# Optimization experiments

Hardware: AMD Instinct MI355X
Metric: run time of the kernel (lower is better)

## Reference

```python
import jax, jax.numpy as jnp
import numpy as np

BLOCK_LEN = 64  # chunk length l


def setup_inputs() -> dict:
    key = jax.random.key(0)
    k1, k2, k3 = jax.random.split(key, 3)
    b, s, h, p, n = 8, 4096, 16, 64, 64
    X = jax.random.normal(k1, (b, s, h, p), jnp.float32)
    # A must be negative for numerically stable decays (exp(cumsum diffs) <= 1),
    # matching real Mamba2 where A_log parameterizes a negative decay rate.
    A = -0.1 * jnp.abs(jax.random.normal(k2, (b, s, h), jnp.float32))
    B = jax.random.normal(k3, (b, s, h, n), jnp.float32)
    return {"X": X, "A": A, "B": B}


def reference(X, A, B):
    L = BLOCK_LEN
    b, s, h, p = X.shape
    n = B.shape[-1]
    c = s // L  # number of chunks

    # b (c l) ... -> b c l ...
    Xb = X.reshape(b, c, L, h, p)
    Bb = B.reshape(b, c, L, h, n)
    Ab = jnp.transpose(A.reshape(b, c, L, h), (0, 3, 1, 2))  # (b, h, c, l)

    A_cumsum = jnp.cumsum(Ab, axis=-1)  # (b, h, c, l)

    # Fused decay-einsum: states[b,c,h,p,n] =
    #   sum_l B[b,c,l,h,n] * exp(A_cumsum[b,h,c,-1] - A_cumsum[b,h,c,l]) * X[b,c,l,h,p]
    decay_states = jnp.exp(A_cumsum[..., -1:] - A_cumsum)  # (b, h, c, l)
    states = jnp.einsum('bclhn,bhcl,bclhp->bchpn', Bb, decay_states, Xb)

    # Prepend zero initial states along chunk dim -> (b, c+1, h, p, n)
    states = jnp.concatenate([jnp.zeros_like(states[:, :1]), states], axis=1)

    # Inter-chunk recurrence via exp(segsum(padded chunk totals)).
    padded_A = jnp.pad(A_cumsum[..., -1], ((0, 0), (0, 0), (1, 0)))  # (b, h, c+1)
    cs = jnp.cumsum(padded_A, axis=-1)
    Z = c + 1
    diff = cs[..., :, None] - cs[..., None, :]  # (b, h, Z, Z), row - col
    mask = jnp.tril(jnp.ones((Z, Z), dtype=bool))  # row >= col
    decay_chunk = jnp.where(mask, jnp.exp(diff), 0.0)  # (b, h, Z, Z)

    new_states = jnp.einsum('bhzc,bchpn->bzhpn', decay_chunk, states)
    return new_states[:, -1]  # (b, h, p, n)
```

## Files before the change

kernel.cpp:

```cpp
#include <hip/hip_runtime.h>
#include <math.h>


constexpr int Bn = 8;
constexpr int S  = 4096;
constexpr int H  = 16;
constexpr int SEG  = 128;
constexpr int NSEG = S / SEG;
constexpr int SC  = 8;
constexpr int TPB = S / SC;
constexpr int TB  = 32;
constexpr int NST = TPB / TB;

#define AS1 __attribute__((address_space(1)))
#define AS3 __attribute__((address_space(3)))

static __device__ __forceinline__ void g2lds16(const float* g, float* l) {
  __builtin_amdgcn_global_load_lds((const AS1 unsigned int*)g, (AS3 unsigned int*)l, 16, 0, 0);
}
static __device__ __forceinline__ void g2lds4(const float* g, float* l) {
  __builtin_amdgcn_global_load_lds((const AS1 unsigned int*)g, (AS3 unsigned int*)l, 4, 0, 0);
}

__global__ __launch_bounds__(256) void scanA(const float* __restrict__ A,
                                             float* __restrict__ Plb,
                                             float* __restrict__ ss) {
  __shared__ float Al[SEG * 17];
  __shared__ float sp[16][17];
  const int bb = blockIdx.x >> 5, seg = blockIdx.x & 31;
  const int tid = threadIdx.x;
  const float* src = A + ((size_t)bb * S + (size_t)seg * SEG) * H;
  #pragma unroll
  for (int k = 0; k < 2; ++k) {
    const int f = tid + k * 256;
    const float4 v = ((const float4*)src)[f];
    const int t = f >> 2, h0 = (f & 3) * 4;
    Al[t * 17 + h0 + 0] = v.x; Al[t * 17 + h0 + 1] = v.y;
    Al[t * 17 + h0 + 2] = v.z; Al[t * 17 + h0 + 3] = v.w;
  }
  __syncthreads();
  const int h = tid >> 4, j = tid & 15;
  float vals[8], run = 0.f;
  #pragma unroll
  for (int k = 0; k < 8; ++k) { run += Al[(j * 8 + k) * 17 + h]; vals[k] = run; }
  sp[h][j] = run;
  __syncthreads();
  float pre = 0.f, tot = 0.f;
  #pragma unroll
  for (int jj = 0; jj < 16; ++jj) { const float x = sp[h][jj]; tot += x; if (jj < j) pre += x; }
  if (j == 0) ss[((size_t)bb * NSEG + seg) * H + h] = tot;
  float* Wp = Plb + ((size_t)(bb * H + h)) * S + seg * SEG + j * 8;
  *(float4*)(Wp)     = make_float4(pre + vals[0], pre + vals[1], pre + vals[2], pre + vals[3]);
  *(float4*)(Wp + 4) = make_float4(pre + vals[4], pre + vals[5], pre + vals[6], pre + vals[7]);
}

__global__ __launch_bounds__(256) void outer_k(const float* __restrict__ X,
                                               const float* __restrict__ Bm,
                                               const float* __restrict__ Plb,
                                               const float* __restrict__ ss,
                                               float* __restrict__ out) {
  __shared__ float smem[4096 + 4096 + 64];
  float* Xs = smem;
  float* Bs = smem + 4096;
  float* Pl = smem + 8192;

  const int blk = blockIdx.x;
  const int pair = blk >> 3, sc = blk & 7;
  const int bb = pair >> 4, hh = pair & 15;
  const int tid = threadIdx.x, w = tid >> 6, lane = tid & 63;
  const int tstart = sc * TPB;
  const int r = lane >> 3, c = lane & 7;

  float segv = (lane < NSEG) ? ss[((size_t)bb * NSEG + lane) * H + hh] : 0.f;
  float incl = segv;
  #pragma unroll
  for (int off = 1; off < NSEG; off <<= 1) {
    const float u = __shfl_up(incl, off, 64);
    if (lane >= off) incl += u;
  }
  const float tot = __shfl(incl, NSEG - 1, 64);
  const float pe  = incl - segv;

  constexpr size_t RS = (size_t)H * 64;
  const float* Xb = X  + (((size_t)bb * S + tstart) * H + hh) * 64;
  const float* Bb = Bm + (((size_t)bb * S + tstart) * H + hh) * 64;
  const float* Pb = Plb + (size_t)pair * S + tstart;

  float acc[8][8];
  #pragma unroll
  for (int i = 0; i < 8; ++i)
    #pragma unroll
    for (int j = 0; j < 8; ++j) acc[i][j] = 0.f;

  #define ISSUE(s_, buf_) do {                                                  \
    const size_t sg = (size_t)(s_) * TB * RS;                                   \
    _Pragma("unroll")                                                           \
    for (int k = 0; k < 2; ++k) {                                               \
      const int i_ = w * 2 + k;                                                 \
      const size_t go = sg + (size_t)(i_ * 4 + (lane >> 4)) * RS                \
                           + (size_t)(lane & 15) * 4;                           \
      g2lds16(Xb + go, Xs + (buf_) * 2048 + i_ * 256);                          \
      g2lds16(Bb + go, Bs + (buf_) * 2048 + i_ * 256);                          \
    }                                                                           \
    if (w == 0 && lane < TB) g2lds4(Pb + (s_) * TB + lane, Pl + (buf_) * 32);   \
  } while (0)

  ISSUE(0, 0);
  for (int s = 0; s < NST; ++s) {
    __syncthreads();
    if (s + 1 < NST) ISSUE(s + 1, (s + 1) & 1);
    const int seg = (tstart + s * TB) >> 7;
    const float cm = tot - __shfl(pe, seg, 64);
    const float* xb = Xs + (s & 1) * 2048;
    const float* bv = Bs + (s & 1) * 2048;
    const float* pl = Pl + (s & 1) * 32;
    #pragma unroll
    for (int it = 0; it < 8; ++it) {
      const int tt = w * 8 + it;
      const float wgt = __expf(cm - pl[tt]);
      const float4 x0 = *(const float4*)(xb + tt * 64 + r * 8);
      const float4 x1 = *(const float4*)(xb + tt * 64 + r * 8 + 4);
      const float4 b0 = *(const float4*)(bv + tt * 64 + c * 8);
      const float4 b1 = *(const float4*)(bv + tt * 64 + c * 8 + 4);
      const float bs[8] = {b0.x * wgt, b0.y * wgt, b0.z * wgt, b0.w * wgt,
                           b1.x * wgt, b1.y * wgt, b1.z * wgt, b1.w * wgt};
      const float xs[8] = {x0.x, x0.y, x0.z, x0.w, x1.x, x1.y, x1.z, x1.w};
      #pragma unroll
      for (int i = 0; i < 8; ++i)
        #pragma unroll
        for (int j = 0; j < 8; ++j)
          acc[i][j] = fmaf(xs[i], bs[j], acc[i][j]);
    }
  }
  __syncthreads();

  float* red = smem;
  if (w >= 2) {
    #pragma unroll
    for (int i = 0; i < 8; ++i)
      #pragma unroll
      for (int j = 0; j < 8; ++j) red[(w - 2) * 4096 + (i * 8 + j) * 64 + lane] = acc[i][j];
  }
  __syncthreads();
  if (w < 2) {
    #pragma unroll
    for (int i = 0; i < 8; ++i)
      #pragma unroll
      for (int j = 0; j < 8; ++j) acc[i][j] += red[w * 4096 + (i * 8 + j) * 64 + lane];
  }
  __syncthreads();
  if (w == 1) {
    #pragma unroll
    for (int i = 0; i < 8; ++i)
      #pragma unroll
      for (int j = 0; j < 8; ++j) red[(i * 8 + j) * 64 + lane] = acc[i][j];
  }
  __syncthreads();
  if (w == 0) {
    float* op = out + (size_t)pair * 4096;
    #pragma unroll
    for (int i = 0; i < 8; ++i)
      #pragma unroll
      for (int j = 0; j < 8; ++j) {
        const float v = acc[i][j] + red[(i * 8 + j) * 64 + lane];
        atomicAdd(&op[(r * 8 + i) * 64 + c * 8 + j], v);
      }
  }
  #undef ISSUE
}

extern "C" void kernel_launch(void* const* d_in, const int* in_sizes, int n_in,
                              void* d_out, int out_size, void* d_ws, size_t ws_size,
                              hipStream_t stream) {
  const float* X = (const float*)d_in[0];
  const float* A = (const float*)d_in[1];
  const float* B = (const float*)d_in[2];
  float* out = (float*)d_out;

  float* Plb = (float*)d_ws;
  float* ss  = Plb + (size_t)Bn * H * S;

  hipMemsetAsync(d_out, 0, (size_t)out_size * sizeof(float), stream);
  scanA<<<Bn * NSEG, 256, 0, stream>>>(A, Plb, ss);
  outer_k<<<Bn * H * SC, 256, 0, stream>>>(X, B, Plb, ss, out);
}
```

Before: 365.6 us.

## Partition output tile across waves instead of time, drop LDS reduction

Each wave now owns a distinct 32x32 quadrant of the 64x64 output with 4x4 accumulators per lane, and iterates over all timesteps of each staged tile. Previously each wave held the full output in an 8x8 register tile over a quarter of the timesteps. That required a multi-stage LDS reduction before the atomics. The grid is doubled (SC 8->16) and the time tile halved, lowering register pressure and raising occupancy. In exchange there are twice as many atomic adds to the output and lower FMA-per-LDS-load reuse.

```diff
diff --git a/kernel.cpp b/kernel.cpp
--- a/kernel.cpp
+++ b/kernel.cpp
@@ -7,9 +7,9 @@
 constexpr int H  = 16;
 constexpr int SEG  = 128;
 constexpr int NSEG = S / SEG;
-constexpr int SC  = 8;
+constexpr int SC  = 16;
 constexpr int TPB = S / SC;
-constexpr int TB  = 32;
+constexpr int TB  = 16;
 constexpr int NST = TPB / TB;
 
 #define AS1 __attribute__((address_space(1)))
@@ -59,17 +59,18 @@
                                                const float* __restrict__ Plb,
                                                const float* __restrict__ ss,
                                                float* __restrict__ out) {
-  __shared__ float smem[4096 + 4096 + 64];
+  __shared__ float smem[2048 + 2048 + 32];
   float* Xs = smem;
-  float* Bs = smem + 4096;
-  float* Pl = smem + 8192;
+  float* Bs = smem + 2048;
+  float* Pl = smem + 4096;
 
   const int blk = blockIdx.x;
-  const int pair = blk >> 3, sc = blk & 7;
+  const int pair = blk >> 4, sc = blk & 15;
   const int bb = pair >> 4, hh = pair & 15;
   const int tid = threadIdx.x, w = tid >> 6, lane = tid & 63;
   const int tstart = sc * TPB;
-  const int r = lane >> 3, c = lane & 7;
+  const int p0 = (w >> 1) * 32 + (lane >> 3) * 4;
+  const int n0 = (w & 1) * 32 + (lane & 7) * 4;
 
   float segv = (lane < NSEG) ? ss[((size_t)bb * NSEG + lane) * H + hh] : 0.f;
   float incl = segv;
@@ -86,23 +87,18 @@
   const float* Bb = Bm + (((size_t)bb * S + tstart) * H + hh) * 64;
   const float* Pb = Plb + (size_t)pair * S + tstart;
 
-  float acc[8][8];
+  float acc[4][4];
   #pragma unroll
-  for (int i = 0; i < 8; ++i)
+  for (int i = 0; i < 4; ++i)
     #pragma unroll
-    for (int j = 0; j < 8; ++j) acc[i][j] = 0.f;
+    for (int j = 0; j < 4; ++j) acc[i][j] = 0.f;
 
   #define ISSUE(s_, buf_) do {                                                  \
-    const size_t sg = (size_t)(s_) * TB * RS;                                   \
-    _Pragma("unroll")                                                           \
-    for (int k = 0; k < 2; ++k) {                                               \
-      const int i_ = w * 2 + k;                                                 \
-      const size_t go = sg + (size_t)(i_ * 4 + (lane >> 4)) * RS                \
-                           + (size_t)(lane & 15) * 4;                           \
-      g2lds16(Xb + go, Xs + (buf_) * 2048 + i_ * 256);                          \
-      g2lds16(Bb + go, Bs + (buf_) * 2048 + i_ * 256);                          \
-    }                                                                           \
-    if (w == 0 && lane < TB) g2lds4(Pb + (s_) * TB + lane, Pl + (buf_) * 32);   \
+    const size_t go = (size_t)((s_) * TB + w * 4 + (lane >> 4)) * RS            \
+                      + (size_t)(lane & 15) * 4;                                \
+    g2lds16(Xb + go, Xs + (buf_) * 1024 + w * 256);                             \
+    g2lds16(Bb + go, Bs + (buf_) * 1024 + w * 256);                             \
+    if (w == 0 && lane < TB) g2lds4(Pb + (s_) * TB + lane, Pl + (buf_) * 16);   \
   } while (0)
 
   ISSUE(0, 0);
@@ -111,61 +107,30 @@
     if (s + 1 < NST) ISSUE(s + 1, (s + 1) & 1);
     const int seg = (tstart + s * TB) >> 7;
     const float cm = tot - __shfl(pe, seg, 64);
-    const float* xb = Xs + (s & 1) * 2048;
-    const float* bv = Bs + (s & 1) * 2048;
-    const float* pl = Pl + (s & 1) * 32;
+    const float* xb = Xs + (s & 1) * 1024;
+    const float* bv = Bs + (s & 1) * 1024;
+    const float* pl = Pl + (s & 1) * 16;
     #pragma unroll
-    for (int it = 0; it < 8; ++it) {
-      const int tt = w * 8 + it;
+    for (int tt = 0; tt < TB; ++tt) {
       const float wgt = __expf(cm - pl[tt]);
-      const float4 x0 = *(const float4*)(xb + tt * 64 + r * 8);
-      const float4 x1 = *(const float4*)(xb + tt * 64 + r * 8 + 4);
-      const float4 b0 = *(const float4*)(bv + tt * 64 + c * 8);
-      const float4 b1 = *(const float4*)(bv + tt * 64 + c * 8 + 4);
-      const float bs[8] = {b0.x * wgt, b0.y * wgt, b0.z * wgt, b0.w * wgt,
-                           b1.x * wgt, b1.y * wgt, b1.z * wgt, b1.w * wgt};
-      const float xs[8] = {x0.x, x0.y, x0.z, x0.w, x1.x, x1.y, x1.z, x1.w};
+      const float4 xv = *(const float4*)(xb + tt * 64 + p0);
+      const float4 b4 = *(const float4*)(bv + tt * 64 + n0);
+      const float bs[4] = {b4.x * wgt, b4.y * wgt, b4.z * wgt, b4.w * wgt};
+      const float xs[4] = {xv.x, xv.y, xv.z, xv.w};
       #pragma unroll
-      for (int i = 0; i < 8; ++i)
+      for (int i = 0; i < 4; ++i)
         #pragma unroll
-        for (int j = 0; j < 8; ++j)
+        for (int j = 0; j < 4; ++j)
           acc[i][j] = fmaf(xs[i], bs[j], acc[i][j]);
     }
   }
-  __syncthreads();
 
-  float* red = smem;
-  if (w >= 2) {
+  float* op = out + (size_t)pair * 4096;
+  #pragma unroll
+  for (int i = 0; i < 4; ++i)
     #pragma unroll
-    for (int i = 0; i < 8; ++i)
-      #pragma unroll
-      for (int j = 0; j < 8; ++j) red[(w - 2) * 4096 + (i * 8 + j) * 64 + lane] = acc[i][j];
-  }
-  __syncthreads();
-  if (w < 2) {
-    #pragma unroll
-    for (int i = 0; i < 8; ++i)
-      #pragma unroll
-      for (int j = 0; j < 8; ++j) acc[i][j] += red[w * 4096 + (i * 8 + j) * 64 + lane];
-  }
-  __syncthreads();
-  if (w == 1) {
-    #pragma unroll
-    for (int i = 0; i < 8; ++i)
-      #pragma unroll
-      for (int j = 0; j < 8; ++j) red[(i * 8 + j) * 64 + lane] = acc[i][j];
-  }
-  __syncthreads();
-  if (w == 0) {
-    float* op = out + (size_t)pair * 4096;
-    #pragma unroll
-    for (int i = 0; i < 8; ++i)
-      #pragma unroll
-      for (int j = 0; j < 8; ++j) {
-        const float v = acc[i][j] + red[(i * 8 + j) * 64 + lane];
-        atomicAdd(&op[(r * 8 + i) * 64 + c * 8 + j], v);
-      }
-  }
+    for (int j = 0; j < 4; ++j)
+      atomicAdd(&op[(size_t)(p0 + i) * 64 + (n0 + j)], acc[i][j]);
   #undef ISSUE
 }
 
```

New measurement: 368.7 us. About the same (+0.9%).
